# Kernel tuning notes

Measured on AMD Instinct MI355X. Metric: run time of the kernel, lower is better.

The kernel has to match this reference:

```python
import jax, jax.numpy as jnp
import numpy as np

VOCAB = 9
D = 128      # EMBED_DIM
S = 64       # SEQ_LEN / context_length
B = 512      # batch
NH = 4       # num_heads
DH = D // NH # head dim = 32
NB = 2       # num_blocks
EPS = 1e-5


def setup_inputs() -> dict:
    key = jax.random.key(0)
    ks = jax.random.split(key, 10)
    rn = lambda k, shape: jax.random.normal(k, shape, jnp.float32) * 0.02
    return {
        "x": jax.random.randint(ks[0], (B, S), 0, VOCAB),
        "emb": rn(ks[1], (VOCAB, D)),
        "ln1_w": jnp.ones((NB, D), jnp.float32),          # pre-sLSTM LayerNorm weight
        "Wg": rn(ks[2], (NB, 4, NH, DH, DH)),             # headwise gate projections (i,f,z,o)
        "R": rn(ks[3], (NB, NH, DH, 4 * DH)),             # recurrent kernels per head
        "bias": rn(ks[4], (NB, NH, 4, DH)),               # cell bias per head/gate
        "gn_w": jnp.ones((NB, D), jnp.float32),           # multi-head (group) norm weight
        "ln2_w": jnp.ones((NB, D), jnp.float32),          # pre-FF LayerNorm weight
        "ff_up_w": rn(ks[5], (NB, 2 * D, D)),             # gated FF up projection
        "ff_down_w": rn(ks[6], (NB, D, D)),               # FF down projection
        "post_w": jnp.ones((D,), jnp.float32),            # post-blocks LayerNorm weight
        "proj_w": rn(ks[7], (VOCAB, D)),
        "proj_b": jnp.zeros((VOCAB,), jnp.float32),
    }


def _layernorm(x, w):
    mu = x.mean(-1, keepdims=True)
    var = x.var(-1, keepdims=True)
    return (x - mu) * jax.lax.rsqrt(var + EPS) * w


def _mh_groupnorm(h, w):
    # h: [B,S,NH,DH] -> normalize over DH per head, scale by per-channel w [D]
    mu = h.mean(-1, keepdims=True)
    var = h.var(-1, keepdims=True)
    hn = (h - mu) * jax.lax.rsqrt(var + EPS)
    return hn.reshape(h.shape[0], h.shape[1], D) * w


def _slstm_layer(xh, Wg, R, b):
    # xh: [B,S,NH,DH]; Wg: [4,NH,DH,DH]; R: [NH,DH,4*DH]; b: [NH,4,DH]
    gx = jnp.einsum('bsnh,gnkh->sbngk', xh, Wg)  # [S,B,NH,4,DH] gate preacts (i,f,z,o)

    def step(carry, g):
        h, c, n, m = carry  # each [B,NH,DH]
        ry = jnp.einsum('bnh,nhk->bnk', h, R).reshape(h.shape[0], NH, 4, DH)
        raw = g + ry + b
        i_r, f_r, z_r, o_r = raw[:, :, 0], raw[:, :, 1], raw[:, :, 2], raw[:, :, 3]
        logfplusm = m + jax.nn.log_sigmoid(f_r)
        mnew = jnp.maximum(i_r, logfplusm)            # stabilizer
        ig = jnp.exp(i_r - mnew)
        fg = jnp.exp(logfplusm - mnew)
        cnew = fg * c + ig * jnp.tanh(z_r)
        nnew = fg * n + ig
        hnew = jax.nn.sigmoid(o_r) * cnew / nnew
        return (hnew, cnew, nnew, mnew), hnew

    z0 = jnp.zeros((xh.shape[0], NH, DH), xh.dtype)
    _, hs = jax.lax.scan(step, (z0, z0, z0, z0), gx)
    return hs.transpose(1, 0, 2, 3)  # [B,S,NH,DH]


def reference(x, emb, ln1_w, Wg, R, bias, gn_w, ln2_w, ff_up_w, ff_down_w, post_w, proj_w, proj_b):
    h = emb[x]  # [B,S,D]
    for bi in range(NB):
        xn = _layernorm(h, ln1_w[bi])
        y = _slstm_layer(xn.reshape(h.shape[0], S, NH, DH), Wg[bi], R[bi], bias[bi])
        h = h + _mh_groupnorm(y, gn_w[bi])
        xn = _layernorm(h, ln2_w[bi])
        up = xn @ ff_up_w[bi].T                       # [B,S,2D]
        gate, upv = up[..., :D], up[..., D:]
        h = h + (jax.nn.gelu(gate, approximate=False) * upv) @ ff_down_w[bi].T
    h = _layernorm(h, post_w)
    return h @ proj_w.T + proj_b  # [B,S,VOCAB]
```

## Files before the change

kernel.cpp:

```cpp
#include <hip/hip_runtime.h>
#include <math.h>

#define D      128
#define S_LEN  64
#define B_SZ   512
#define NH     4
#define DH     32
#define NB     2
#define VOCAB  9
#define EPS    1e-5f
#define NTOK   (B_SZ * S_LEN)

template <int CTRL>
__device__ __forceinline__ float dppf(float x) {
    return __int_as_float(__builtin_amdgcn_update_dpp(
        0, __float_as_int(x), CTRL, 0xF, 0xF, true));
}
__device__ __forceinline__ float wsum64(float x) {
    x += dppf<0x111>(x);
    x += dppf<0x112>(x);
    x += dppf<0x114>(x);
    x += dppf<0x118>(x);
    x += dppf<0x142>(x);
    x += dppf<0x143>(x);
    return __int_as_float(__builtin_amdgcn_readlane(__float_as_int(x), 63));
}

__device__ __forceinline__ int xc3(int t, int c) { return c ^ (((t >> 1) & 7) << 2); }
__device__ __forceinline__ int xa (int t, int c) { return c ^ ((t & 7) << 2); }
__device__ __forceinline__ int xg (int c)        { return c ^ ((c >> 5) << 3); }

__global__ __launch_bounds__(256) void k_embed(const int* __restrict__ x,
                                               const float* __restrict__ emb,
                                               float* __restrict__ h,
                                               float* __restrict__ stats)
{
    int lane = threadIdx.x & 63;
    int wv   = threadIdx.x >> 6;
    int tok  = blockIdx.x * 4 + wv;
    int xi   = x[tok];
    float2 v = ((const float2*)(emb + xi * D))[lane];
    ((float2*)(h + (size_t)tok * D))[lane] = v;
    float s1 = wsum64(v.x + v.y);
    float s2 = wsum64(v.x * v.x + v.y * v.y);
    float mu  = s1 * (1.0f / D);
    float var = s2 * (1.0f / D) - mu * mu;
    if (lane == 0) {
        stats[tok * 2]     = mu;
        stats[tok * 2 + 1] = rsqrtf(var + EPS);
    }
}

__global__ __launch_bounds__(256, 2) void k_gx(const float* __restrict__ Wg,
                                               const float* __restrict__ bias,
                                               const float* __restrict__ lnw,
                                               const float* __restrict__ h,
                                               const float* __restrict__ stats,
                                               float* __restrict__ gx)
{
    __shared__ float xs[32 * 128];
    __shared__ float wl[4 * 32 * 128];

    int tid  = threadIdx.x;
    int lane = tid & 63;
    int wv   = tid >> 6;
    size_t tok0 = (size_t)blockIdx.x * 32;

    {
        int q = tid & 7;
        #pragma unroll
        for (int it = 0; it < 16; ++it) {
            int row = it * 32 + (tid >> 3);
            int g  = row >> 7;
            int n  = (row >> 5) & 3;
            int hh = row & 31;
            float4 v = *(const float4*)(Wg + row * 32 + q * 4);
            int col = g * 32 + hh;
            int sw  = q << 2;
            float* dst = wl + n * 4096;
            dst[(q * 4 + 0) * 128 + (col ^ sw)] = v.x;
            dst[(q * 4 + 1) * 128 + (col ^ sw)] = v.y;
            dst[(q * 4 + 2) * 128 + (col ^ sw)] = v.z;
            dst[(q * 4 + 3) * 128 + (col ^ sw)] = v.w;
        }
    }
    for (int i = 0; i < 8; ++i) {
        int t = wv * 8 + i;
        const float* hp = h + (tok0 + t) * D;
        float mu = stats[(tok0 + t) * 2];
        float rs = stats[(tok0 + t) * 2 + 1];
        float v1 = (hp[lane]      - mu) * rs * lnw[lane];
        float v2 = (hp[64 + lane] - mu) * rs * lnw[64 + lane];
        xs[t * 128 + xg(lane)]      = v1;
        xs[t * 128 + xg(lane + 64)] = v2;
    }
    __syncthreads();

    int nh   = lane >> 4;
    int col0 = (lane & 15) * 8;
    int t0   = wv * 8;

    float acc[8][8];
    #pragma unroll
    for (int j = 0; j < 8; ++j)
        #pragma unroll
        for (int cc = 0; cc < 8; ++cc) acc[j][cc] = 0.f;

    const float* wbase = wl + nh * 4096;
    #pragma unroll 4
    for (int k = 0; k < 32; ++k) {
        int sw = (k >> 2) << 2;
        float4 w0 = *(const float4*)&wbase[k * 128 + (col0 ^ sw)];
        float4 w1 = *(const float4*)&wbase[k * 128 + ((col0 + 4) ^ sw)];
        int ac = (nh * 32 + k) ^ (nh << 3);
        #pragma unroll
        for (int j = 0; j < 8; ++j) {
            float a = xs[(t0 + j) * 128 + ac];
            acc[j][0] = fmaf(a, w0.x, acc[j][0]);
            acc[j][1] = fmaf(a, w0.y, acc[j][1]);
            acc[j][2] = fmaf(a, w0.z, acc[j][2]);
            acc[j][3] = fmaf(a, w0.w, acc[j][3]);
            acc[j][4] = fmaf(a, w1.x, acc[j][4]);
            acc[j][5] = fmaf(a, w1.y, acc[j][5]);
            acc[j][6] = fmaf(a, w1.z, acc[j][6]);
            acc[j][7] = fmaf(a, w1.w, acc[j][7]);
        }
    }

    float4 bb0 = *(const float4*)(bias + nh * 128 + col0);
    float4 bb1 = *(const float4*)(bias + nh * 128 + col0 + 4);
    #pragma unroll
    for (int j = 0; j < 8; ++j) {
        int gt = (int)tok0 + t0 + j;
        int bb = gt >> 6;
        int ss = gt & 63;
        float* op = gx + ((size_t)(bb * NH + nh) * S_LEN + ss) * 128 + col0;
        float4 o0v, o1v;
        o0v.x = acc[j][0] + bb0.x; o0v.y = acc[j][1] + bb0.y;
        o0v.z = acc[j][2] + bb0.z; o0v.w = acc[j][3] + bb0.w;
        o1v.x = acc[j][4] + bb1.x; o1v.y = acc[j][5] + bb1.y;
        o1v.z = acc[j][6] + bb1.z; o1v.w = acc[j][7] + bb1.w;
        *(float4*)op       = o0v;
        *(float4*)(op + 4) = o1v;
    }
}

__global__ __launch_bounds__(64, 1) void k_scan(const float* __restrict__ Rm,
                                                const float* __restrict__ gnw,
                                                const float* __restrict__ gx,
                                                float* __restrict__ h)
{
    __shared__ float WA[8][64][4];
    __shared__ float WB[8][64][4];

    int b    = blockIdx.x >> 2;
    int n    = blockIdx.x & 3;
    int lane = threadIdx.x;
    int e    = lane >> 1;
    int sub  = lane & 1;
    int colA = sub * DH + e;

    #pragma unroll
    for (int cc = 0; cc < 8; ++cc) {
        float4 a, bv;
        #pragma unroll
        for (int j = 0; j < 4; ++j) {
            ((float*)&a)[j]  = Rm[(n * DH + cc * 4 + j) * 128 + colA];
            ((float*)&bv)[j] = Rm[(n * DH + cc * 4 + j) * 128 + 64 + colA];
        }
        *(float4*)WA[cc][lane] = a;
        *(float4*)WB[cc][lane] = bv;
    }
    float gw = gnw[n * DH + e];
    __syncthreads();

    float c = 0.f, nacc = 0.f, m = 0.f;
    float hu[DH];
    #pragma unroll
    for (int i = 0; i < DH; ++i) hu[i] = 0.f;

    float* hb = h + ((size_t)b * S_LEN) * D + n * DH;
    const float* gxp = gx + ((size_t)(b * NH + n) * S_LEN) * 128;

    float pGA[4], pGB[4], pHR[4];
    #pragma unroll
    for (int k = 0; k < 4; ++k) {
        pGA[k] = gxp[k * 128 + colA];
        pGB[k] = gxp[k * 128 + 64 + colA];
        pHR[k] = hb[k * D + e];
    }

    #pragma unroll 4
    for (int s = 0; s < S_LEN; ++s) {
        int sp = (s + 4 < S_LEN) ? s + 4 : S_LEN - 1;
        float nGA = gxp[sp * 128 + colA];
        float nGB = gxp[sp * 128 + 64 + colA];
        float nHR = hb[sp * D + e];

        float r0=0,r1=0,r2=0,r3=0,q0=0,q1=0,q2=0,q3=0;
        #pragma unroll
        for (int cc = 0; cc < 8; ++cc) {
            float4 wa = *(const float4*)WA[cc][lane];
            float4 wb = *(const float4*)WB[cc][lane];
            r0 = fmaf(hu[cc*4+0], wa.x, r0);
            r1 = fmaf(hu[cc*4+1], wa.y, r1);
            r2 = fmaf(hu[cc*4+2], wa.z, r2);
            r3 = fmaf(hu[cc*4+3], wa.w, r3);
            q0 = fmaf(hu[cc*4+0], wb.x, q0);
            q1 = fmaf(hu[cc*4+1], wb.y, q1);
            q2 = fmaf(hu[cc*4+2], wb.z, q2);
            q3 = fmaf(hu[cc*4+3], wb.w, q3);
        }
        float rawA = pGA[0] + ((r0 + r1) + (r2 + r3));
        float rawB = pGB[0] + ((q0 + q1) + (q2 + q3));

        float xA = dppf<0xB1>(rawA);
        float xB = dppf<0xB1>(rawB);
        float i_r = sub ? xA   : rawA;
        float f_r = sub ? rawA : xA;
        float z_r = sub ? xB   : rawB;
        float o_r = sub ? rawB : xB;

        float lsf  = fminf(f_r, 0.f)
                   - 0.69314718055994531f * __log2f(1.0f + __expf(-fabsf(f_r)));
        float lfm  = m + lsf;
        float mnew = fmaxf(i_r, lfm);
        float ig   = __expf(i_r - mnew);
        float fg   = __expf(lfm - mnew);
        float t    = __expf(2.f * z_r);
        float tz   = 1.f - 2.f / (t + 1.f);
        c    = fg * c + ig * tz;
        nacc = fg * nacc + ig;
        m    = mnew;
        float hv = c / (nacc * (1.f + __expf(-o_r)));

        float s1 = wsum64(hv);
        float s2 = wsum64(hv * hv);
        float mu  = s1 * (1.f / 64.f);
        float var = s2 * (1.f / 64.f) - mu * mu;
        float hn  = (hv - mu) * rsqrtf(var + EPS) * gw;

        if (!sub) hb[s * D + e] = pHR[0] + hn;

        #pragma unroll
        for (int i = 0; i < DH; ++i)
            hu[i] = __int_as_float(
                __builtin_amdgcn_readlane(__float_as_int(hv), 2 * i));

        pGA[0]=pGA[1]; pGA[1]=pGA[2]; pGA[2]=pGA[3]; pGA[3]=nGA;
        pGB[0]=pGB[1]; pGB[1]=pGB[2]; pGB[2]=pGB[3]; pGB[3]=nGB;
        pHR[0]=pHR[1]; pHR[1]=pHR[2]; pHR[2]=pHR[3]; pHR[3]=nHR;
    }
}

template <int LAST>
__global__ __launch_bounds__(256, 2) void k_ff(float* __restrict__ h,
                                               const float* __restrict__ ln2w,
                                               const float* __restrict__ wup,
                                               const float* __restrict__ wdn,
                                               float* __restrict__ stats_out,
                                               const float* __restrict__ lastw,
                                               const float* __restrict__ projw,
                                               const float* __restrict__ projb,
                                               float* __restrict__ out)
{
    __shared__ float xs[32 * 128];
    __shared__ float as_[32 * 64];
    __shared__ float wt[2 * 32 * 64];

    int tid  = threadIdx.x;
    int lane = tid & 63;
    int wv   = tid >> 6;
    size_t tok0 = (size_t)blockIdx.x * 32;

    for (int i = 0; i < 8; ++i) {
        int t = wv * 8 + i;
        const float* hp = h + (tok0 + t) * D;
        float v1 = hp[lane], v2 = hp[64 + lane];
        float s1 = wsum64(v1 + v2);
        float s2 = wsum64(v1 * v1 + v2 * v2);
        float mu = s1 * (1.0f / D);
        float rs = rsqrtf(s2 * (1.0f / D) - mu * mu + EPS);
        xs[t * D + xc3(t, lane)]      = (v1 - mu) * rs * ln2w[lane];
        xs[t * D + xc3(t, lane + 64)] = (v2 - mu) * rs * ln2w[64 + lane];
    }

    int q     = tid & 7;
    int r0    = tid >> 3;
    int goff0 = r0 * D + q * 4;
    int goff1 = (r0 + 32) * D + q * 4;
    int s0    = r0 ^ (q << 2);
    int kb    = q * 4;

    auto ffld = [&](int id, float4* pre) {
        int p = (id >= 6) ? 1 : 0;
        int j = id - p * 6;
        const float* b0;
        const float* b1;
        if (j < 4) { b0 = wup + (p * 64) * D + j * 32;
                     b1 = wup + (128 + p * 64) * D + j * 32; }
        else       { int jj = j - 4;
                     b0 = wdn + p * 64 + jj * 32;
                     b1 = wdn + 64 * D + p * 64 + jj * 32; }
        pre[0] = *(const float4*)(b0 + goff0);
        pre[1] = *(const float4*)(b0 + goff1);
        pre[2] = *(const float4*)(b1 + goff0);
        pre[3] = *(const float4*)(b1 + goff1);
    };
    auto fst = [&](const float4* pre) {
        #pragma unroll
        for (int cc = 0; cc < 4; ++cc) {
            const float* p0 = (const float*)&pre[0];
            const float* p1 = (const float*)&pre[1];
            const float* p2 = (const float*)&pre[2];
            const float* p3 = (const float*)&pre[3];
            wt[(kb + cc) * 64 + s0]           = p0[cc];
            wt[(kb + cc) * 64 + s0 + 32]      = p1[cc];
            wt[2048 + (kb + cc) * 64 + s0]      = p2[cc];
            wt[2048 + (kb + cc) * 64 + s0 + 32] = p3[cc];
        }
    };

    int ti = tid >> 4;
    int oi = tid & 15;
    int t0 = ti * 2;
    int o0 = oi * 4;

    float accd[2][2][4];
    #pragma unroll
    for (int a1 = 0; a1 < 2; ++a1)
        #pragma unroll
        for (int j = 0; j < 2; ++j)
            #pragma unroll
            for (int cc = 0; cc < 4; ++cc) accd[a1][j][cc] = 0.f;

    float4 pre[4];
    ffld(0, pre);
    int id = 1;

    #pragma unroll
    for (int p = 0; p < 2; ++p) {
        float accg[2][4], accv[2][4];
        #pragma unroll
        for (int j = 0; j < 2; ++j)
            #pragma unroll
            for (int cc = 0; cc < 4; ++cc) { accg[j][cc] = 0.f; accv[j][cc] = 0.f; }

        for (int c4 = 0; c4 < 4; ++c4) {
            __syncthreads();
            fst(pre);
            if (id < 12) ffld(id, pre);
            ++id;
            __syncthreads();
            int kc = c4 * 32;
            #pragma unroll
            for (int k4 = 0; k4 < 8; ++k4) {
                float4 a0 = *(const float4*)&xs[t0 * D + xc3(t0, kc + k4 * 4)];
                float4 a1v = *(const float4*)&xs[(t0 + 1) * D + xc3(t0 + 1, kc + k4 * 4)];
                int ws = k4 << 2;
                #pragma unroll
                for (int i = 0; i < 4; ++i) {
                    int k = k4 * 4 + i;
                    float4 bg = *(const float4*)&wt[k * 64 + (o0 ^ ws)];
                    float4 bv = *(const float4*)&wt[2048 + k * 64 + (o0 ^ ws)];
                    float ax0 = ((const float*)&a0)[i];
                    float ax1 = ((const float*)&a1v)[i];
                    accg[0][0] = fmaf(ax0, bg.x, accg[0][0]);
                    accg[0][1] = fmaf(ax0, bg.y, accg[0][1]);
                    accg[0][2] = fmaf(ax0, bg.z, accg[0][2]);
                    accg[0][3] = fmaf(ax0, bg.w, accg[0][3]);
                    accg[1][0] = fmaf(ax1, bg.x, accg[1][0]);
                    accg[1][1] = fmaf(ax1, bg.y, accg[1][1]);
                    accg[1][2] = fmaf(ax1, bg.z, accg[1][2]);
                    accg[1][3] = fmaf(ax1, bg.w, accg[1][3]);
                    accv[0][0] = fmaf(ax0, bv.x, accv[0][0]);
                    accv[0][1] = fmaf(ax0, bv.y, accv[0][1]);
                    accv[0][2] = fmaf(ax0, bv.z, accv[0][2]);
                    accv[0][3] = fmaf(ax0, bv.w, accv[0][3]);
                    accv[1][0] = fmaf(ax1, bv.x, accv[1][0]);
                    accv[1][1] = fmaf(ax1, bv.y, accv[1][1]);
                    accv[1][2] = fmaf(ax1, bv.z, accv[1][2]);
                    accv[1][3] = fmaf(ax1, bv.w, accv[1][3]);
                }
            }
        }
        #pragma unroll
        for (int j = 0; j < 2; ++j) {
            int t = t0 + j;
            float4 av;
            float* ap = (float*)&av;
            #pragma unroll
            for (int cc = 0; cc < 4; ++cc) {
                float g = accg[j][cc];
                float u = accv[j][cc];
                ap[cc] = 0.5f * g * (1.0f + erff(g * 0.70710678118654752f)) * u;
            }
            *(float4*)&as_[t * 64 + xa(t, o0)] = av;
        }
        for (int c2 = 0; c2 < 2; ++c2) {
            __syncthreads();
            fst(pre);
            if (id < 12) ffld(id, pre);
            ++id;
            __syncthreads();
            int kc = c2 * 32;
            #pragma unroll
            for (int k4 = 0; k4 < 8; ++k4) {
                float4 a0 = *(const float4*)&as_[t0 * 64 + xa(t0, kc + k4 * 4)];
                float4 a1v = *(const float4*)&as_[(t0 + 1) * 64 + xa(t0 + 1, kc + k4 * 4)];
                int ws = k4 << 2;
                #pragma unroll
                for (int i = 0; i < 4; ++i) {
                    int k = k4 * 4 + i;
                    float4 b0v = *(const float4*)&wt[k * 64 + (o0 ^ ws)];
                    float4 b1v = *(const float4*)&wt[2048 + k * 64 + (o0 ^ ws)];
                    float ax0 = ((const float*)&a0)[i];
                    float ax1 = ((const float*)&a1v)[i];
                    accd[0][0][0] = fmaf(ax0, b0v.x, accd[0][0][0]);
                    accd[0][0][1] = fmaf(ax0, b0v.y, accd[0][0][1]);
                    accd[0][0][2] = fmaf(ax0, b0v.z, accd[0][0][2]);
                    accd[0][0][3] = fmaf(ax0, b0v.w, accd[0][0][3]);
                    accd[0][1][0] = fmaf(ax1, b0v.x, accd[0][1][0]);
                    accd[0][1][1] = fmaf(ax1, b0v.y, accd[0][1][1]);
                    accd[0][1][2] = fmaf(ax1, b0v.z, accd[0][1][2]);
                    accd[0][1][3] = fmaf(ax1, b0v.w, accd[0][1][3]);
                    accd[1][0][0] = fmaf(ax0, b1v.x, accd[1][0][0]);
                    accd[1][0][1] = fmaf(ax0, b1v.y, accd[1][0][1]);
                    accd[1][0][2] = fmaf(ax0, b1v.z, accd[1][0][2]);
                    accd[1][0][3] = fmaf(ax0, b1v.w, accd[1][0][3]);
                    accd[1][1][0] = fmaf(ax1, b1v.x, accd[1][1][0]);
                    accd[1][1][1] = fmaf(ax1, b1v.y, accd[1][1][1]);
                    accd[1][1][2] = fmaf(ax1, b1v.z, accd[1][1][2]);
                    accd[1][1][3] = fmaf(ax1, b1v.w, accd[1][1][3]);
                }
            }
        }
    }

    #pragma unroll
    for (int j = 0; j < 2; ++j) {
        int t = t0 + j;
        size_t tok = tok0 + t;
        #pragma unroll
        for (int a1 = 0; a1 < 2; ++a1) {
            int cb = a1 * 64 + o0;
            float4 hres = *(const float4*)(h + tok * D + cb);
            float4 hn;
            hn.x = hres.x + accd[a1][j][0];
            hn.y = hres.y + accd[a1][j][1];
            hn.z = hres.z + accd[a1][j][2];
            hn.w = hres.w + accd[a1][j][3];
            if (!LAST) *(float4*)(h + tok * D + cb) = hn;
            *(float4*)&xs[t * D + xc3(t, cb)] = hn;
        }
    }
    __syncthreads();

    if (!LAST) {
        for (int i = 0; i < 8; ++i) {
            int t = wv * 8 + i;
            float v1 = xs[t * D + xc3(t, lane)];
            float v2 = xs[t * D + xc3(t, lane + 64)];
            float s1 = wsum64(v1 + v2);
            float s2 = wsum64(v1 * v1 + v2 * v2);
            float mu = s1 * (1.0f / D);
            float rs = rsqrtf(s2 * (1.0f / D) - mu * mu + EPS);
            if (lane == 0) {
                stats_out[(tok0 + t) * 2]     = mu;
                stats_out[(tok0 + t) * 2 + 1] = rs;
            }
        }
    } else {
        float pw1[VOCAB], pw2[VOCAB], pb[VOCAB];
        #pragma unroll
        for (int v = 0; v < VOCAB; ++v) {
            pw1[v] = projw[v * D + lane];
            pw2[v] = projw[v * D + 64 + lane];
            pb[v]  = projb[v];
        }
        for (int i = 0; i < 8; ++i) {
            int t = wv * 8 + i;
            float v1 = xs[t * D + xc3(t, lane)];
            float v2 = xs[t * D + xc3(t, lane + 64)];
            float s1 = wsum64(v1 + v2);
            float s2 = wsum64(v1 * v1 + v2 * v2);
            float mu = s1 * (1.0f / D);
            float rs = rsqrtf(s2 * (1.0f / D) - mu * mu + EPS);
            float x1 = (v1 - mu) * rs * lastw[lane];
            float x2 = (v2 - mu) * rs * lastw[64 + lane];
            #pragma unroll
            for (int v = 0; v < VOCAB; ++v) {
                float pp = wsum64(fmaf(x1, pw1[v], x2 * pw2[v]));
                if (lane == 0) out[(tok0 + t) * VOCAB + v] = pp + pb[v];
            }
        }
    }
}

extern "C" void kernel_launch(void* const* d_in, const int* in_sizes, int n_in,
                              void* d_out, int out_size, void* d_ws, size_t ws_size,
                              hipStream_t stream)
{
    const int*   x     = (const int*)  d_in[0];
    const float* emb   = (const float*)d_in[1];
    const float* ln1   = (const float*)d_in[2];
    const float* Wg    = (const float*)d_in[3];
    const float* Rm    = (const float*)d_in[4];
    const float* bias  = (const float*)d_in[5];
    const float* gnw   = (const float*)d_in[6];
    const float* ln2   = (const float*)d_in[7];
    const float* wup   = (const float*)d_in[8];
    const float* wdn   = (const float*)d_in[9];
    const float* postw = (const float*)d_in[10];
    const float* projw = (const float*)d_in[11];
    const float* projb = (const float*)d_in[12];
    float* out   = (float*)d_out;
    float* hbuf  = (float*)d_ws;
    float* stats = hbuf + (size_t)NTOK * D;
    float* gxbuf = stats + (size_t)NTOK * 2;

    k_embed<<<NTOK / 4, 256, 0, stream>>>(x, emb, hbuf, stats);

    for (int bi = 0; bi < NB; ++bi) {
        k_gx<<<NTOK / 32, 256, 0, stream>>>(Wg + bi * 4 * NH * DH * DH,
                                            bias + bi * NH * 4 * DH,
                                            ln1 + bi * D,
                                            hbuf, stats, gxbuf);
        k_scan<<<B_SZ * NH, 64, 0, stream>>>(Rm + bi * NH * DH * 4 * DH,
                                             gnw + bi * D,
                                             gxbuf, hbuf);
        if (bi == 0)
            k_ff<0><<<NTOK / 32, 256, 0, stream>>>(hbuf, ln2 + bi * D,
                                                   wup + bi * 2 * D * D,
                                                   wdn + bi * D * D,
                                                   stats, nullptr, nullptr,
                                                   nullptr, nullptr);
        else
            k_ff<1><<<NTOK / 32, 256, 0, stream>>>(hbuf, ln2 + bi * D,
                                                   wup + bi * 2 * D * D,
                                                   wdn + bi * D * D,
                                                   nullptr, postw, projw,
                                                   projb, out);
    }
}
```

Before: 386.0 us.

## Restructure FF kernel with 64-token tiles, 4x4 register blocking, and LDS-direct weight loads

The feed-forward kernel now processes 64 tokens per block instead of 32, with each thread computing a 4-token by 4-output tile. The up-projection computes all 256 outputs in one pass rather than two halves. Weights are copied straight from global memory into LDS with global_load_lds, replacing the register prefetch-and-store path. The aim is more FMAs per shared-memory load and fewer global weight fetches per token, at the cost of more registers, more LDS, and no overlap between weight loading and compute.

New measurement: 395.7 us. 2.5% more time.

```diff
diff --git a/kernel.cpp b/kernel.cpp
--- a/kernel.cpp
+++ b/kernel.cpp
@@ -26,9 +26,25 @@
     return __int_as_float(__builtin_amdgcn_readlane(__float_as_int(x), 63));
 }
 
-__device__ __forceinline__ int xc3(int t, int c) { return c ^ (((t >> 1) & 7) << 2); }
-__device__ __forceinline__ int xa (int t, int c) { return c ^ ((t & 7) << 2); }
 __device__ __forceinline__ int xg (int c)        { return c ^ ((c >> 5) << 3); }
+
+__device__ __forceinline__ void gl16(const float* g, float* l) {
+    __builtin_amdgcn_global_load_lds(
+        (const __attribute__((address_space(1))) void*)g,
+        (__attribute__((address_space(3))) void*)l, 16, 0, 0);
+}
+
+__device__ __forceinline__ float dot4(float4 a, float4 b, float c) {
+    c = fmaf(a.x, b.x, c);
+    c = fmaf(a.y, b.y, c);
+    c = fmaf(a.z, b.z, c);
+    c = fmaf(a.w, b.w, c);
+    return c;
+}
+
+__device__ __forceinline__ float gelu_exact(float g) {
+    return 0.5f * g * (1.0f + erff(g * 0.70710678118654752f));
+}
 
 __global__ __launch_bounds__(256) void k_embed(const int* __restrict__ x,
                                                const float* __restrict__ emb,
@@ -254,213 +270,188 @@
 }
 
 template <int LAST>
-__global__ __launch_bounds__(256, 2) void k_ff(float* __restrict__ h,
-                                               const float* __restrict__ ln2w,
-                                               const float* __restrict__ wup,
-                                               const float* __restrict__ wdn,
-                                               float* __restrict__ stats_out,
-                                               const float* __restrict__ lastw,
-                                               const float* __restrict__ projw,
-                                               const float* __restrict__ projb,
-                                               float* __restrict__ out)
+__global__ __launch_bounds__(256) void k_ff(float* __restrict__ h,
+                                            const float* __restrict__ ln2w,
+                                            const float* __restrict__ wup,
+                                            const float* __restrict__ wdn,
+                                            float* __restrict__ stats_out,
+                                            const float* __restrict__ lastw,
+                                            const float* __restrict__ projw,
+                                            const float* __restrict__ projb,
+                                            float* __restrict__ out)
 {
-    __shared__ float xs[32 * 128];
-    __shared__ float as_[32 * 64];
-    __shared__ float wt[2 * 32 * 64];
+    __shared__ float xs[64 * 128];
+    __shared__ float wt[128 * 64];
 
     int tid  = threadIdx.x;
     int lane = tid & 63;
     int wv   = tid >> 6;
-    size_t tok0 = (size_t)blockIdx.x * 32;
-
-    for (int i = 0; i < 8; ++i) {
-        int t = wv * 8 + i;
+    int oi   = lane & 15;
+    int ti   = lane >> 4;
+    int tg   = wv * 4 + ti;
+    int t0   = tg * 4;
+    int swv  = oi & 7;
+    int swt  = tg & 7;
+    size_t tok0 = (size_t)blockIdx.x * 64;
+
+    for (int i = 0; i < 16; ++i) {
+        int t = wv * 16 + i;
         const float* hp = h + (tok0 + t) * D;
         float v1 = hp[lane], v2 = hp[64 + lane];
         float s1 = wsum64(v1 + v2);
         float s2 = wsum64(v1 * v1 + v2 * v2);
         float mu = s1 * (1.0f / D);
         float rs = rsqrtf(s2 * (1.0f / D) - mu * mu + EPS);
-        xs[t * D + xc3(t, lane)]      = (v1 - mu) * rs * ln2w[lane];
-        xs[t * D + xc3(t, lane + 64)] = (v2 - mu) * rs * ln2w[64 + lane];
-    }
-
-    int q     = tid & 7;
-    int r0    = tid >> 3;
-    int goff0 = r0 * D + q * 4;
-    int goff1 = (r0 + 32) * D + q * 4;
-    int s0    = r0 ^ (q << 2);
-    int kb    = q * 4;
-
-    auto ffld = [&](int id, float4* pre) {
-        int p = (id >= 6) ? 1 : 0;
-        int j = id - p * 6;
-        const float* b0;
-        const float* b1;
-        if (j < 4) { b0 = wup + (p * 64) * D + j * 32;
-                     b1 = wup + (128 + p * 64) * D + j * 32; }
-        else       { int jj = j - 4;
-                     b0 = wdn + p * 64 + jj * 32;
-                     b1 = wdn + 64 * D + p * 64 + jj * 32; }
-        pre[0] = *(const float4*)(b0 + goff0);
-        pre[1] = *(const float4*)(b0 + goff1);
-        pre[2] = *(const float4*)(b1 + goff0);
-        pre[3] = *(const float4*)(b1 + goff1);
-    };
-    auto fst = [&](const float4* pre) {
-        #pragma unroll
-        for (int cc = 0; cc < 4; ++cc) {
-            const float* p0 = (const float*)&pre[0];
-            const float* p1 = (const float*)&pre[1];
-            const float* p2 = (const float*)&pre[2];
-            const float* p3 = (const float*)&pre[3];
-            wt[(kb + cc) * 64 + s0]           = p0[cc];
-            wt[(kb + cc) * 64 + s0 + 32]      = p1[cc];
-            wt[2048 + (kb + cc) * 64 + s0]      = p2[cc];
-            wt[2048 + (kb + cc) * 64 + s0 + 32] = p3[cc];
-        }
-    };
-
-    int ti = tid >> 4;
-    int oi = tid & 15;
-    int t0 = ti * 2;
-    int o0 = oi * 4;
-
-    float accd[2][2][4];
-    #pragma unroll
-    for (int a1 = 0; a1 < 2; ++a1)
-        #pragma unroll
-        for (int j = 0; j < 2; ++j)
+        int sx = ((t >> 2) & 7) << 2;
+        xs[t * 128 + (lane ^ sx)]        = (v1 - mu) * rs * ln2w[lane];
+        xs[t * 128 + ((lane + 64) ^ sx)] = (v2 - mu) * rs * ln2w[64 + lane];
+    }
+
+    float ag0[4][4], ag1[4][4], av0[4][4], av1[4][4];
+    #pragma unroll
+    for (int a = 0; a < 4; ++a)
+        #pragma unroll
+        for (int j = 0; j < 4; ++j) { ag0[a][j]=0.f; ag1[a][j]=0.f; av0[a][j]=0.f; av1[a][j]=0.f; }
+
+    for (int c4 = 0; c4 < 4; ++c4) {
+        int kc = c4 * 32;
+        __syncthreads();
+        #pragma unroll
+        for (int q = 0; q < 8; ++q) {
+            int r  = (q * 4 + wv) * 4 + (lane >> 4);
+            int s  = lane & 15;
+            int o  = r + ((s >> 3) << 7);
+            int sl = (s & 7) ^ ((r >> 2) & 7);
+            gl16(wup + o * 128 + kc + (sl << 2), wt + (q * 4 + wv) * 256);
+        }
+        __syncthreads();
+
+        #pragma unroll 2
+        for (int k4 = 0; k4 < 8; ++k4) {
+            int ac = (((c4 * 8 + k4) ^ swt) << 2);
+            float4 a0 = *(const float4*)&xs[(t0 + 0) * 128 + ac];
+            float4 a1 = *(const float4*)&xs[(t0 + 1) * 128 + ac];
+            float4 a2 = *(const float4*)&xs[(t0 + 2) * 128 + ac];
+            float4 a3 = *(const float4*)&xs[(t0 + 3) * 128 + ac];
+            int ks = (k4 ^ swv) << 2;
             #pragma unroll
-            for (int cc = 0; cc < 4; ++cc) accd[a1][j][cc] = 0.f;
-
-    float4 pre[4];
-    ffld(0, pre);
-    int id = 1;
-
-    #pragma unroll
-    for (int p = 0; p < 2; ++p) {
-        float accg[2][4], accv[2][4];
-        #pragma unroll
-        for (int j = 0; j < 2; ++j)
+            for (int j = 0; j < 4; ++j) {
+                const float* wrl = wt + (oi * 4 + j) * 64;
+                const float* wrh = wrl + 64 * 64;
+                float4 bgl = *(const float4*)&wrl[ks];
+                float4 bvl = *(const float4*)&wrl[32 + ks];
+                float4 bgh = *(const float4*)&wrh[ks];
+                float4 bvh = *(const float4*)&wrh[32 + ks];
+                ag0[0][j] = dot4(a0, bgl, ag0[0][j]);
+                ag0[1][j] = dot4(a1, bgl, ag0[1][j]);
+                ag0[2][j] = dot4(a2, bgl, ag0[2][j]);
+                ag0[3][j] = dot4(a3, bgl, ag0[3][j]);
+                av0[0][j] = dot4(a0, bvl, av0[0][j]);
+                av0[1][j] = dot4(a1, bvl, av0[1][j]);
+                av0[2][j] = dot4(a2, bvl, av0[2][j]);
+                av0[3][j] = dot4(a3, bvl, av0[3][j]);
+                ag1[0][j] = dot4(a0, bgh, ag1[0][j]);
+                ag1[1][j] = dot4(a1, bgh, ag1[1][j]);
+                ag1[2][j] = dot4(a2, bgh, ag1[2][j]);
+                ag1[3][j] = dot4(a3, bgh, ag1[3][j]);
+                av1[0][j] = dot4(a0, bvh, av1[0][j]);
+                av1[1][j] = dot4(a1, bvh, av1[1][j]);
+                av1[2][j] = dot4(a2, bvh, av1[2][j]);
+                av1[3][j] = dot4(a3, bvh, av1[3][j]);
+            }
+        }
+    }
+
+    __syncthreads();
+
+    #pragma unroll
+    for (int tt = 0; tt < 4; ++tt) {
+        int t = t0 + tt;
+        float4 lo, hi;
+        lo.x = gelu_exact(ag0[tt][0]) * av0[tt][0];
+        lo.y = gelu_exact(ag0[tt][1]) * av0[tt][1];
+        lo.z = gelu_exact(ag0[tt][2]) * av0[tt][2];
+        lo.w = gelu_exact(ag0[tt][3]) * av0[tt][3];
+        hi.x = gelu_exact(ag1[tt][0]) * av1[tt][0];
+        hi.y = gelu_exact(ag1[tt][1]) * av1[tt][1];
+        hi.z = gelu_exact(ag1[tt][2]) * av1[tt][2];
+        hi.w = gelu_exact(ag1[tt][3]) * av1[tt][3];
+        int sb = (oi ^ swt) << 2;
+        *(float4*)&xs[t * 128 + sb]      = lo;
+        *(float4*)&xs[t * 128 + 64 + sb] = hi;
+    }
+
+    float ad0[4][4], ad1[4][4];
+    #pragma unroll
+    for (int a = 0; a < 4; ++a)
+        #pragma unroll
+        for (int j = 0; j < 4; ++j) { ad0[a][j]=0.f; ad1[a][j]=0.f; }
+
+    for (int ch = 0; ch < 2; ++ch) {
+        int cc = ch * 64;
+        #pragma unroll
+        for (int q = 0; q < 8; ++q) {
+            int r  = (q * 4 + wv) * 4 + (lane >> 4);
+            int s  = lane & 15;
+            int sl = s ^ ((r >> 2) & 7);
+            gl16(wdn + r * 128 + cc + (sl << 2), wt + (q * 4 + wv) * 256);
+        }
+        __syncthreads();
+
+        #pragma unroll 4
+        for (int u4 = 0; u4 < 16; ++u4) {
+            int ac = (((ch * 16 + u4) ^ swt) << 2);
+            float4 a0 = *(const float4*)&xs[(t0 + 0) * 128 + ac];
+            float4 a1 = *(const float4*)&xs[(t0 + 1) * 128 + ac];
+            float4 a2 = *(const float4*)&xs[(t0 + 2) * 128 + ac];
+            float4 a3 = *(const float4*)&xs[(t0 + 3) * 128 + ac];
+            int ks = (u4 ^ swv) << 2;
             #pragma unroll
-            for (int cc = 0; cc < 4; ++cc) { accg[j][cc] = 0.f; accv[j][cc] = 0.f; }
-
-        for (int c4 = 0; c4 < 4; ++c4) {
-            __syncthreads();
-            fst(pre);
-            if (id < 12) ffld(id, pre);
-            ++id;
-            __syncthreads();
-            int kc = c4 * 32;
-            #pragma unroll
-            for (int k4 = 0; k4 < 8; ++k4) {
-                float4 a0 = *(const float4*)&xs[t0 * D + xc3(t0, kc + k4 * 4)];
-                float4 a1v = *(const float4*)&xs[(t0 + 1) * D + xc3(t0 + 1, kc + k4 * 4)];
-                int ws = k4 << 2;
-                #pragma unroll
-                for (int i = 0; i < 4; ++i) {
-                    int k = k4 * 4 + i;
-                    float4 bg = *(const float4*)&wt[k * 64 + (o0 ^ ws)];
-                    float4 bv = *(const float4*)&wt[2048 + k * 64 + (o0 ^ ws)];
-                    float ax0 = ((const float*)&a0)[i];
-                    float ax1 = ((const float*)&a1v)[i];
-                    accg[0][0] = fmaf(ax0, bg.x, accg[0][0]);
-                    accg[0][1] = fmaf(ax0, bg.y, accg[0][1]);
-                    accg[0][2] = fmaf(ax0, bg.z, accg[0][2]);
-                    accg[0][3] = fmaf(ax0, bg.w, accg[0][3]);
-                    accg[1][0] = fmaf(ax1, bg.x, accg[1][0]);
-                    accg[1][1] = fmaf(ax1, bg.y, accg[1][1]);
-                    accg[1][2] = fmaf(ax1, bg.z, accg[1][2]);
-                    accg[1][3] = fmaf(ax1, bg.w, accg[1][3]);
-                    accv[0][0] = fmaf(ax0, bv.x, accv[0][0]);
-                    accv[0][1] = fmaf(ax0, bv.y, accv[0][1]);
-                    accv[0][2] = fmaf(ax0, bv.z, accv[0][2]);
-                    accv[0][3] = fmaf(ax0, bv.w, accv[0][3]);
-                    accv[1][0] = fmaf(ax1, bv.x, accv[1][0]);
-                    accv[1][1] = fmaf(ax1, bv.y, accv[1][1]);
-                    accv[1][2] = fmaf(ax1, bv.z, accv[1][2]);
-                    accv[1][3] = fmaf(ax1, bv.w, accv[1][3]);
-                }
+            for (int j = 0; j < 4; ++j) {
+                const float* wrl = wt + (oi * 4 + j) * 64;
+                const float* wrh = wrl + 64 * 64;
+                float4 b0 = *(const float4*)&wrl[ks];
+                float4 b1 = *(const float4*)&wrh[ks];
+                ad0[0][j] = dot4(a0, b0, ad0[0][j]);
+                ad0[1][j] = dot4(a1, b0, ad0[1][j]);
+                ad0[2][j] = dot4(a2, b0, ad0[2][j]);
+                ad0[3][j] = dot4(a3, b0, ad0[3][j]);
+                ad1[0][j] = dot4(a0, b1, ad1[0][j]);
+                ad1[1][j] = dot4(a1, b1, ad1[1][j]);
+                ad1[2][j] = dot4(a2, b1, ad1[2][j]);
+                ad1[3][j] = dot4(a3, b1, ad1[3][j]);
             }
         }
-        #pragma unroll
-        for (int j = 0; j < 2; ++j) {
-            int t = t0 + j;
-            float4 av;
-            float* ap = (float*)&av;
-            #pragma unroll
-            for (int cc = 0; cc < 4; ++cc) {
-                float g = accg[j][cc];
-                float u = accv[j][cc];
-                ap[cc] = 0.5f * g * (1.0f + erff(g * 0.70710678118654752f)) * u;
-            }
-            *(float4*)&as_[t * 64 + xa(t, o0)] = av;
-        }
-        for (int c2 = 0; c2 < 2; ++c2) {
-            __syncthreads();
-            fst(pre);
-            if (id < 12) ffld(id, pre);
-            ++id;
-            __syncthreads();
-            int kc = c2 * 32;
-            #pragma unroll
-            for (int k4 = 0; k4 < 8; ++k4) {
-                float4 a0 = *(const float4*)&as_[t0 * 64 + xa(t0, kc + k4 * 4)];
-                float4 a1v = *(const float4*)&as_[(t0 + 1) * 64 + xa(t0 + 1, kc + k4 * 4)];
-                int ws = k4 << 2;
-                #pragma unroll
-                for (int i = 0; i < 4; ++i) {
-                    int k = k4 * 4 + i;
-                    float4 b0v = *(const float4*)&wt[k * 64 + (o0 ^ ws)];
-                    float4 b1v = *(const float4*)&wt[2048 + k * 64 + (o0 ^ ws)];
-                    float ax0 = ((const float*)&a0)[i];
-                    float ax1 = ((const float*)&a1v)[i];
-                    accd[0][0][0] = fmaf(ax0, b0v.x, accd[0][0][0]);
-                    accd[0][0][1] = fmaf(ax0, b0v.y, accd[0][0][1]);
-                    accd[0][0][2] = fmaf(ax0, b0v.z, accd[0][0][2]);
-                    accd[0][0][3] = fmaf(ax0, b0v.w, accd[0][0][3]);
-                    accd[0][1][0] = fmaf(ax1, b0v.x, accd[0][1][0]);
-                    accd[0][1][1] = fmaf(ax1, b0v.y, accd[0][1][1]);
-                    accd[0][1][2] = fmaf(ax1, b0v.z, accd[0][1][2]);
-                    accd[0][1][3] = fmaf(ax1, b0v.w, accd[0][1][3]);
-                    accd[1][0][0] = fmaf(ax0, b1v.x, accd[1][0][0]);
-                    accd[1][0][1] = fmaf(ax0, b1v.y, accd[1][0][1]);
-                    accd[1][0][2] = fmaf(ax0, b1v.z, accd[1][0][2]);
-                    accd[1][0][3] = fmaf(ax0, b1v.w, accd[1][0][3]);
-                    accd[1][1][0] = fmaf(ax1, b1v.x, accd[1][1][0]);
-                    accd[1][1][1] = fmaf(ax1, b1v.y, accd[1][1][1]);
-                    accd[1][1][2] = fmaf(ax1, b1v.z, accd[1][1][2]);
-                    accd[1][1][3] = fmaf(ax1, b1v.w, accd[1][1][3]);
-                }
-            }
-        }
-    }
-
-    #pragma unroll
-    for (int j = 0; j < 2; ++j) {
-        int t = t0 + j;
+        __syncthreads();
+    }
+
+    #pragma unroll
+    for (int tt = 0; tt < 4; ++tt) {
+        int t = t0 + tt;
         size_t tok = tok0 + t;
-        #pragma unroll
-        for (int a1 = 0; a1 < 2; ++a1) {
-            int cb = a1 * 64 + o0;
-            float4 hres = *(const float4*)(h + tok * D + cb);
-            float4 hn;
-            hn.x = hres.x + accd[a1][j][0];
-            hn.y = hres.y + accd[a1][j][1];
-            hn.z = hres.z + accd[a1][j][2];
-            hn.w = hres.w + accd[a1][j][3];
-            if (!LAST) *(float4*)(h + tok * D + cb) = hn;
-            *(float4*)&xs[t * D + xc3(t, cb)] = hn;
-        }
+        float4 r0v = *(const float4*)(h + tok * D + oi * 4);
+        float4 r1v = *(const float4*)(h + tok * D + 64 + oi * 4);
+        float4 h0, h1;
+        h0.x = r0v.x + ad0[tt][0]; h0.y = r0v.y + ad0[tt][1];
+        h0.z = r0v.z + ad0[tt][2]; h0.w = r0v.w + ad0[tt][3];
+        h1.x = r1v.x + ad1[tt][0]; h1.y = r1v.y + ad1[tt][1];
+        h1.z = r1v.z + ad1[tt][2]; h1.w = r1v.w + ad1[tt][3];
+        if (!LAST) {
+            *(float4*)(h + tok * D + oi * 4)      = h0;
+            *(float4*)(h + tok * D + 64 + oi * 4) = h1;
+        }
+        int sb = (oi ^ swt) << 2;
+        *(float4*)&xs[t * 128 + sb]      = h0;
+        *(float4*)&xs[t * 128 + 64 + sb] = h1;
     }
     __syncthreads();
 
     if (!LAST) {
-        for (int i = 0; i < 8; ++i) {
-            int t = wv * 8 + i;
-            float v1 = xs[t * D + xc3(t, lane)];
-            float v2 = xs[t * D + xc3(t, lane + 64)];
+        for (int i = 0; i < 16; ++i) {
+            int t = wv * 16 + i;
+            int sx = ((t >> 2) & 7) << 2;
+            float v1 = xs[t * 128 + (lane ^ sx)];
+            float v2 = xs[t * 128 + ((lane + 64) ^ sx)];
             float s1 = wsum64(v1 + v2);
             float s2 = wsum64(v1 * v1 + v2 * v2);
             float mu = s1 * (1.0f / D);
@@ -478,10 +469,11 @@
             pw2[v] = projw[v * D + 64 + lane];
             pb[v]  = projb[v];
         }
-        for (int i = 0; i < 8; ++i) {
-            int t = wv * 8 + i;
-            float v1 = xs[t * D + xc3(t, lane)];
-            float v2 = xs[t * D + xc3(t, lane + 64)];
+        for (int i = 0; i < 16; ++i) {
+            int t = wv * 16 + i;
+            int sx = ((t >> 2) & 7) << 2;
+            float v1 = xs[t * 128 + (lane ^ sx)];
+            float v2 = xs[t * 128 + ((lane + 64) ^ sx)];
             float s1 = wsum64(v1 + v2);
             float s2 = wsum64(v1 * v1 + v2 * v2);
             float mu = s1 * (1.0f / D);
@@ -530,13 +522,13 @@
                                              gnw + bi * D,
                                              gxbuf, hbuf);
         if (bi == 0)
-            k_ff<0><<<NTOK / 32, 256, 0, stream>>>(hbuf, ln2 + bi * D,
+            k_ff<0><<<NTOK / 64, 256, 0, stream>>>(hbuf, ln2 + bi * D,
                                                    wup + bi * 2 * D * D,
                                                    wdn + bi * D * D,
                                                    stats, nullptr, nullptr,
                                                    nullptr, nullptr);
         else
-            k_ff<1><<<NTOK / 32, 256, 0, stream>>>(hbuf, ln2 + bi * D,
+            k_ff<1><<<NTOK / 64, 256, 0, stream>>>(hbuf, ln2 + bi * D,
                                                    wup + bi * 2 * D * D,
                                                    wdn + bi * D * D,
                                                    nullptr, postw, projw,
```

## Halve FF block threads and give each thread four tokens per tile

Applied to the files above, without the earlier changes.

The feed-forward kernel now runs 128 threads per block instead of 256. Each thread computes four tokens by four outputs instead of two by four, so every weight value read from shared memory feeds twice as many FMAs. Weight staging and the layernorm loops are reworked to match, and the activation swizzle is changed to avoid bank conflicts under the new per-thread token pattern. The larger per-thread tile raises register pressure and leaves fewer waves per block to hide latency.

New measurement: 389.4 us. Within noise of the previous version (+0.9%).

```diff
diff --git a/kernel.cpp b/kernel.cpp
--- a/kernel.cpp
+++ b/kernel.cpp
@@ -27,8 +27,14 @@
 }
 
 __device__ __forceinline__ int xc3(int t, int c) { return c ^ (((t >> 1) & 7) << 2); }
-__device__ __forceinline__ int xa (int t, int c) { return c ^ ((t & 7) << 2); }
+__device__ __forceinline__ int xa2(int t, int c) {
+    return c ^ (((((t >> 2) * 5) + (t & 3)) & 7) << 2);
+}
 __device__ __forceinline__ int xg (int c)        { return c ^ ((c >> 5) << 3); }
+
+__device__ __forceinline__ float gelu_exact(float g) {
+    return 0.5f * g * (1.0f + erff(g * 0.70710678118654752f));
+}
 
 __global__ __launch_bounds__(256) void k_embed(const int* __restrict__ x,
                                                const float* __restrict__ emb,
@@ -254,7 +260,7 @@
 }
 
 template <int LAST>
-__global__ __launch_bounds__(256, 2) void k_ff(float* __restrict__ h,
+__global__ __launch_bounds__(128, 2) void k_ff(float* __restrict__ h,
                                                const float* __restrict__ ln2w,
                                                const float* __restrict__ wup,
                                                const float* __restrict__ wdn,
@@ -273,8 +279,8 @@
     int wv   = tid >> 6;
     size_t tok0 = (size_t)blockIdx.x * 32;
 
-    for (int i = 0; i < 8; ++i) {
-        int t = wv * 8 + i;
+    for (int i = 0; i < 16; ++i) {
+        int t = wv * 16 + i;
         const float* hp = h + (tok0 + t) * D;
         float v1 = hp[lane], v2 = hp[64 + lane];
         float s1 = wsum64(v1 + v2);
@@ -285,12 +291,9 @@
         xs[t * D + xc3(t, lane + 64)] = (v2 - mu) * rs * ln2w[64 + lane];
     }
 
-    int q     = tid & 7;
-    int r0    = tid >> 3;
-    int goff0 = r0 * D + q * 4;
-    int goff1 = (r0 + 32) * D + q * 4;
-    int s0    = r0 ^ (q << 2);
-    int kb    = q * 4;
+    int q  = tid & 7;
+    int r0 = tid >> 3;
+    int kb = q * 4;
 
     auto ffld = [&](int id, float4* pre) {
         int p = (id >= 6) ? 1 : 0;
@@ -302,49 +305,60 @@
         else       { int jj = j - 4;
                      b0 = wdn + p * 64 + jj * 32;
                      b1 = wdn + 64 * D + p * 64 + jj * 32; }
-        pre[0] = *(const float4*)(b0 + goff0);
-        pre[1] = *(const float4*)(b0 + goff1);
-        pre[2] = *(const float4*)(b1 + goff0);
-        pre[3] = *(const float4*)(b1 + goff1);
+        #pragma unroll
+        for (int u = 0; u < 2; ++u) {
+            int ru = r0 + u * 16;
+            int g0 = ru * D + q * 4;
+            int g1 = (ru + 32) * D + q * 4;
+            pre[u * 4 + 0] = *(const float4*)(b0 + g0);
+            pre[u * 4 + 1] = *(const float4*)(b0 + g1);
+            pre[u * 4 + 2] = *(const float4*)(b1 + g0);
+            pre[u * 4 + 3] = *(const float4*)(b1 + g1);
+        }
     };
     auto fst = [&](const float4* pre) {
         #pragma unroll
-        for (int cc = 0; cc < 4; ++cc) {
-            const float* p0 = (const float*)&pre[0];
-            const float* p1 = (const float*)&pre[1];
-            const float* p2 = (const float*)&pre[2];
-            const float* p3 = (const float*)&pre[3];
-            wt[(kb + cc) * 64 + s0]           = p0[cc];
-            wt[(kb + cc) * 64 + s0 + 32]      = p1[cc];
-            wt[2048 + (kb + cc) * 64 + s0]      = p2[cc];
-            wt[2048 + (kb + cc) * 64 + s0 + 32] = p3[cc];
+        for (int u = 0; u < 2; ++u) {
+            int ru = r0 + u * 16;
+            int su = ru ^ (q << 2);
+            #pragma unroll
+            for (int cc = 0; cc < 4; ++cc) {
+                const float* p0 = (const float*)&pre[u * 4 + 0];
+                const float* p1 = (const float*)&pre[u * 4 + 1];
+                const float* p2 = (const float*)&pre[u * 4 + 2];
+                const float* p3 = (const float*)&pre[u * 4 + 3];
+                wt[(kb + cc) * 64 + su]             = p0[cc];
+                wt[(kb + cc) * 64 + su + 32]        = p1[cc];
+                wt[2048 + (kb + cc) * 64 + su]      = p2[cc];
+                wt[2048 + (kb + cc) * 64 + su + 32] = p3[cc];
+            }
         }
     };
 
     int ti = tid >> 4;
     int oi = tid & 15;
-    int t0 = ti * 2;
+    int t0 = ti * 4;
     int o0 = oi * 4;
 
-    float accd[2][2][4];
+    float accd[2][4][4];
     #pragma unroll
     for (int a1 = 0; a1 < 2; ++a1)
         #pragma unroll
-        for (int j = 0; j < 2; ++j)
+        for (int tt = 0; tt < 4; ++tt)
             #pragma unroll
-            for (int cc = 0; cc < 4; ++cc) accd[a1][j][cc] = 0.f;
-
-    float4 pre[4];
+            for (int cc = 0; cc < 4; ++cc) accd[a1][tt][cc] = 0.f;
+
+    float4 pre[8];
     ffld(0, pre);
     int id = 1;
 
     #pragma unroll
     for (int p = 0; p < 2; ++p) {
-        float accg[2][4], accv[2][4];
-        #pragma unroll
-        for (int j = 0; j < 2; ++j)
+        float accg[4][4], accv[4][4];
+        #pragma unroll
+        for (int tt = 0; tt < 4; ++tt)
             #pragma unroll
-            for (int cc = 0; cc < 4; ++cc) { accg[j][cc] = 0.f; accv[j][cc] = 0.f; }
+            for (int cc = 0; cc < 4; ++cc) { accg[tt][cc] = 0.f; accv[tt][cc] = 0.f; }
 
         for (int c4 = 0; c4 < 4; ++c4) {
             __syncthreads();
@@ -353,49 +367,42 @@
             ++id;
             __syncthreads();
             int kc = c4 * 32;
-            #pragma unroll
+            #pragma unroll 2
             for (int k4 = 0; k4 < 8; ++k4) {
-                float4 a0 = *(const float4*)&xs[t0 * D + xc3(t0, kc + k4 * 4)];
-                float4 a1v = *(const float4*)&xs[(t0 + 1) * D + xc3(t0 + 1, kc + k4 * 4)];
+                float4 a[4];
+                #pragma unroll
+                for (int tt = 0; tt < 4; ++tt)
+                    a[tt] = *(const float4*)&xs[(t0 + tt) * D + xc3(t0 + tt, kc + k4 * 4)];
                 int ws = k4 << 2;
                 #pragma unroll
                 for (int i = 0; i < 4; ++i) {
                     int k = k4 * 4 + i;
                     float4 bg = *(const float4*)&wt[k * 64 + (o0 ^ ws)];
                     float4 bv = *(const float4*)&wt[2048 + k * 64 + (o0 ^ ws)];
-                    float ax0 = ((const float*)&a0)[i];
-                    float ax1 = ((const float*)&a1v)[i];
-                    accg[0][0] = fmaf(ax0, bg.x, accg[0][0]);
-                    accg[0][1] = fmaf(ax0, bg.y, accg[0][1]);
-                    accg[0][2] = fmaf(ax0, bg.z, accg[0][2]);
-                    accg[0][3] = fmaf(ax0, bg.w, accg[0][3]);
-                    accg[1][0] = fmaf(ax1, bg.x, accg[1][0]);
-                    accg[1][1] = fmaf(ax1, bg.y, accg[1][1]);
-                    accg[1][2] = fmaf(ax1, bg.z, accg[1][2]);
-                    accg[1][3] = fmaf(ax1, bg.w, accg[1][3]);
-                    accv[0][0] = fmaf(ax0, bv.x, accv[0][0]);
-                    accv[0][1] = fmaf(ax0, bv.y, accv[0][1]);
-                    accv[0][2] = fmaf(ax0, bv.z, accv[0][2]);
-                    accv[0][3] = fmaf(ax0, bv.w, accv[0][3]);
-                    accv[1][0] = fmaf(ax1, bv.x, accv[1][0]);
-                    accv[1][1] = fmaf(ax1, bv.y, accv[1][1]);
-                    accv[1][2] = fmaf(ax1, bv.z, accv[1][2]);
-                    accv[1][3] = fmaf(ax1, bv.w, accv[1][3]);
+                    #pragma unroll
+                    for (int tt = 0; tt < 4; ++tt) {
+                        float ax = ((const float*)&a[tt])[i];
+                        accg[tt][0] = fmaf(ax, bg.x, accg[tt][0]);
+                        accg[tt][1] = fmaf(ax, bg.y, accg[tt][1]);
+                        accg[tt][2] = fmaf(ax, bg.z, accg[tt][2]);
+                        accg[tt][3] = fmaf(ax, bg.w, accg[tt][3]);
+                        accv[tt][0] = fmaf(ax, bv.x, accv[tt][0]);
+                        accv[tt][1] = fmaf(ax, bv.y, accv[tt][1]);
+                        accv[tt][2] = fmaf(ax, bv.z, accv[tt][2]);
+                        accv[tt][3] = fmaf(ax, bv.w, accv[tt][3]);
+                    }
                 }
             }
         }
         #pragma unroll
-        for (int j = 0; j < 2; ++j) {
-            int t = t0 + j;
+        for (int tt = 0; tt < 4; ++tt) {
+            int t = t0 + tt;
             float4 av;
             float* ap = (float*)&av;
             #pragma unroll
-            for (int cc = 0; cc < 4; ++cc) {
-                float g = accg[j][cc];
-                float u = accv[j][cc];
-                ap[cc] = 0.5f * g * (1.0f + erff(g * 0.70710678118654752f)) * u;
-            }
-            *(float4*)&as_[t * 64 + xa(t, o0)] = av;
+            for (int cc = 0; cc < 4; ++cc)
+                ap[cc] = gelu_exact(accg[tt][cc]) * accv[tt][cc];
+            *(float4*)&as_[t * 64 + xa2(t, o0)] = av;
         }
         for (int c2 = 0; c2 < 2; ++c2) {
             __syncthreads();
@@ -404,52 +411,48 @@
             ++id;
             __syncthreads();
             int kc = c2 * 32;
-            #pragma unroll
+            #pragma unroll 2
             for (int k4 = 0; k4 < 8; ++k4) {
-                float4 a0 = *(const float4*)&as_[t0 * 64 + xa(t0, kc + k4 * 4)];
-                float4 a1v = *(const float4*)&as_[(t0 + 1) * 64 + xa(t0 + 1, kc + k4 * 4)];
+                float4 a[4];
+                #pragma unroll
+                for (int tt = 0; tt < 4; ++tt)
+                    a[tt] = *(const float4*)&as_[(t0 + tt) * 64 + xa2(t0 + tt, kc + k4 * 4)];
                 int ws = k4 << 2;
                 #pragma unroll
                 for (int i = 0; i < 4; ++i) {
                     int k = k4 * 4 + i;
                     float4 b0v = *(const float4*)&wt[k * 64 + (o0 ^ ws)];
                     float4 b1v = *(const float4*)&wt[2048 + k * 64 + (o0 ^ ws)];
-                    float ax0 = ((const float*)&a0)[i];
-                    float ax1 = ((const float*)&a1v)[i];
-                    accd[0][0][0] = fmaf(ax0, b0v.x, accd[0][0][0]);
-                    accd[0][0][1] = fmaf(ax0, b0v.y, accd[0][0][1]);
-                    accd[0][0][2] = fmaf(ax0, b0v.z, accd[0][0][2]);
-                    accd[0][0][3] = fmaf(ax0, b0v.w, accd[0][0][3]);
-                    accd[0][1][0] = fmaf(ax1, b0v.x, accd[0][1][0]);
-                    accd[0][1][1] = fmaf(ax1, b0v.y, accd[0][1][1]);
-                    accd[0][1][2] = fmaf(ax1, b0v.z, accd[0][1][2]);
-                    accd[0][1][3] = fmaf(ax1, b0v.w, accd[0][1][3]);
-                    accd[1][0][0] = fmaf(ax0, b1v.x, accd[1][0][0]);
-                    accd[1][0][1] = fmaf(ax0, b1v.y, accd[1][0][1]);
-                    accd[1][0][2] = fmaf(ax0, b1v.z, accd[1][0][2]);
-                    accd[1][0][3] = fmaf(ax0, b1v.w, accd[1][0][3]);
-                    accd[1][1][0] = fmaf(ax1, b1v.x, accd[1][1][0]);
-                    accd[1][1][1] = fmaf(ax1, b1v.y, accd[1][1][1]);
-                    accd[1][1][2] = fmaf(ax1, b1v.z, accd[1][1][2]);
-                    accd[1][1][3] = fmaf(ax1, b1v.w, accd[1][1][3]);
+                    #pragma unroll
+                    for (int tt = 0; tt < 4; ++tt) {
+                        float ax = ((const float*)&a[tt])[i];
+                        accd[0][tt][0] = fmaf(ax, b0v.x, accd[0][tt][0]);
+                        accd[0][tt][1] = fmaf(ax, b0v.y, accd[0][tt][1]);
+                        accd[0][tt][2] = fmaf(ax, b0v.z, accd[0][tt][2]);
+                        accd[0][tt][3] = fmaf(ax, b0v.w, accd[0][tt][3]);
+                        accd[1][tt][0] = fmaf(ax, b1v.x, accd[1][tt][0]);
+                        accd[1][tt][1] = fmaf(ax, b1v.y, accd[1][tt][1]);
+                        accd[1][tt][2] = fmaf(ax, b1v.z, accd[1][tt][2]);
+                        accd[1][tt][3] = fmaf(ax, b1v.w, accd[1][tt][3]);
+                    }
                 }
             }
         }
     }
 
     #pragma unroll
-    for (int j = 0; j < 2; ++j) {
-        int t = t0 + j;
+    for (int tt = 0; tt < 4; ++tt) {
+        int t = t0 + tt;
         size_t tok = tok0 + t;
         #pragma unroll
         for (int a1 = 0; a1 < 2; ++a1) {
             int cb = a1 * 64 + o0;
             float4 hres = *(const float4*)(h + tok * D + cb);
             float4 hn;
-            hn.x = hres.x + accd[a1][j][0];
-            hn.y = hres.y + accd[a1][j][1];
-            hn.z = hres.z + accd[a1][j][2];
-            hn.w = hres.w + accd[a1][j][3];
+            hn.x = hres.x + accd[a1][tt][0];
+            hn.y = hres.y + accd[a1][tt][1];
+            hn.z = hres.z + accd[a1][tt][2];
+            hn.w = hres.w + accd[a1][tt][3];
             if (!LAST) *(float4*)(h + tok * D + cb) = hn;
             *(float4*)&xs[t * D + xc3(t, cb)] = hn;
         }
@@ -457,8 +460,8 @@
     __syncthreads();
 
     if (!LAST) {
-        for (int i = 0; i < 8; ++i) {
-            int t = wv * 8 + i;
+        for (int i = 0; i < 16; ++i) {
+            int t = wv * 16 + i;
             float v1 = xs[t * D + xc3(t, lane)];
             float v2 = xs[t * D + xc3(t, lane + 64)];
             float s1 = wsum64(v1 + v2);
@@ -478,8 +481,8 @@
             pw2[v] = projw[v * D + 64 + lane];
             pb[v]  = projb[v];
         }
-        for (int i = 0; i < 8; ++i) {
-            int t = wv * 8 + i;
+        for (int i = 0; i < 16; ++i) {
+            int t = wv * 16 + i;
             float v1 = xs[t * D + xc3(t, lane)];
             float v2 = xs[t * D + xc3(t, lane + 64)];
             float s1 = wsum64(v1 + v2);
@@ -530,13 +533,13 @@
                                              gnw + bi * D,
                                              gxbuf, hbuf);
         if (bi == 0)
-            k_ff<0><<<NTOK / 32, 256, 0, stream>>>(hbuf, ln2 + bi * D,
+            k_ff<0><<<NTOK / 32, 128, 0, stream>>>(hbuf, ln2 + bi * D,
                                                    wup + bi * 2 * D * D,
                                                    wdn + bi * D * D,
                                                    stats, nullptr, nullptr,
                                                    nullptr, nullptr);
         else
-            k_ff<1><<<NTOK / 32, 256, 0, stream>>>(hbuf, ln2 + bi * D,
+            k_ff<1><<<NTOK / 32, 128, 0, stream>>>(hbuf, ln2 + bi * D,
                                                    wup + bi * 2 * D * D,
                                                    wdn + bi * D * D,
                                                    nullptr, postw, projw,
```
